# Kernel optimization log

Measured on AMD Instinct MI355X. Metric: run time of the kernel, lower is better.

## Reference

```python
import jax, jax.numpy as jnp
import numpy as np

TEMPERATURE = 8.0  # sqrt(d_k) with d_k = 64
MASK_FILL = -65504.0  # fp16 min, as in the original


def setup_inputs() -> dict:
    key = jax.random.key(0)
    kq, kk, kv, km = jax.random.split(key, 4)
    BH, L, D = 16, 2048, 64
    q = jax.random.normal(kq, (BH, L, D), dtype=jnp.float32)
    k = jax.random.normal(kk, (BH, L, D), dtype=jnp.float32)
    v = jax.random.normal(kv, (BH, L, D), dtype=jnp.float32)
    mask = jax.random.randint(km, (BH, L, L), 0, 2).astype(jnp.bool_)
    return {"q": q, "k": k, "v": v, "mask": mask}


def reference(q, k, v, mask):
    # attn = q @ k^T / temperature, masked_fill, softmax over last dim
    attn = jnp.einsum("bqd,bkd->bqk", q, k) / TEMPERATURE
    attn = jnp.where(mask, MASK_FILL, attn)
    attn = jax.nn.softmax(attn, axis=2)
    # dropout with p=0.0 is identity (eval-mode reference)
    output = jnp.einsum("bqk,bkd->bqd", attn, v)
    return (output, attn)
```

## Files before the change

kernel.cpp:

```cpp
#include <hip/hip_runtime.h>

#define BH 16
#define L 2048
#define D 64
#define QB 32
#define KB 64
#define NKT (L / KB)
#define SCALE 0.125f
#define MASK_FILL -65504.0f

typedef __bf16 bf16x8 __attribute__((ext_vector_type(8)));
typedef float f32x4 __attribute__((ext_vector_type(4)));

__device__ __forceinline__ unsigned f2bf(float f) {
    union { float f; unsigned u; } x; x.f = f;
    return (x.u + 0x7FFFu + ((x.u >> 16) & 1u)) >> 16;
}
__device__ __forceinline__ float bf2f(unsigned short h) {
    union { unsigned u; float f; } x; x.u = ((unsigned)h) << 16;
    return x.f;
}


extern "C" __global__ __launch_bounds__(256)
void preK(const float* __restrict__ k, uint4* __restrict__ wsK)
{
    int idx = blockIdx.x * 256 + threadIdx.x;
    int c   = idx & 7;
    int key = (idx >> 3) & (L - 1);
    int bh  = idx >> 14;
    const float4* src = (const float4*)(k + ((size_t)(bh * L + key) * D + c * 8));
    float4 a = src[0], b = src[1];
    uint4 o;
    o.x = f2bf(a.x) | (f2bf(a.y) << 16);
    o.y = f2bf(a.z) | (f2bf(a.w) << 16);
    o.z = f2bf(b.x) | (f2bf(b.y) << 16);
    o.w = f2bf(b.z) | (f2bf(b.w) << 16);
    wsK[(size_t)(bh * L + key) * 8 + (c ^ (key & 7))] = o;
}

extern "C" __global__ __launch_bounds__(256)
void preV(const float* __restrict__ v, uint4* __restrict__ wsVt)
{
    __shared__ float sT[64 * 68];
    int b = blockIdx.x;
    int bh = b >> 5, kt = b & 31;
    const float4* src = (const float4*)(v + ((size_t)bh * L + kt * 64) * D);
    int t = threadIdx.x;
    #pragma unroll
    for (int i = 0; i < 4; ++i) {
        int i4 = i * 256 + t;
        int key = i4 >> 4, c4 = i4 & 15;
        float4 val = src[i4];
        *(float4*)&sT[key * 68 + c4 * 4] = val;
    }
    __syncthreads();
    int d = t >> 2, cg = t & 3;
    #pragma unroll
    for (int j = 0; j < 2; ++j) {
        int c = cg + j * 4;
        unsigned pk[4];
        #pragma unroll
        for (int e = 0; e < 4; ++e) {
            float x0 = sT[(c * 8 + e * 2    ) * 68 + d];
            float x1 = sT[(c * 8 + e * 2 + 1) * 68 + d];
            pk[e] = f2bf(x0) | (f2bf(x1) << 16);
        }
        wsVt[((size_t)(bh * 32 + kt) * 64 + d) * 8 + (c ^ (d & 7))] =
            make_uint4(pk[0], pk[1], pk[2], pk[3]);
    }
}

extern "C" __global__ __launch_bounds__(256)
void preM(const int* __restrict__ mask, unsigned long long* __restrict__ wsM)
{
    __shared__ unsigned long long sW[16 * 32];
    int b = blockIdx.x;
    size_t row0 = (size_t)b * 16;
    int w = threadIdx.x >> 6, lane = threadIdx.x & 63;
    const int* src = mask + row0 * L;
    for (int rr = 0; rr < 4; ++rr) {
        int r = w * 4 + rr;
        #pragma unroll 8
        for (int wd = 0; wd < 32; ++wd) {
            int val = src[(size_t)r * L + wd * 64 + lane];
            unsigned long long bal = __ballot(val != 0);
            if (lane == 0) sW[r * 32 + wd] = bal;
        }
    }
    __syncthreads();
    int t = threadIdx.x;
    ((uint4*)wsM)[(size_t)b * 256 + t] = ((const uint4*)sW)[t];
}


extern "C" __global__ __launch_bounds__(256, 4)
void sdpa_main(const float* __restrict__ q, const uint4* __restrict__ gKall,
               const uint4* __restrict__ gVall, const unsigned long long* __restrict__ wsM,
               float* __restrict__ out, float* __restrict__ attn)
{
    __shared__ unsigned short sP[2][QB * 72];
    __shared__ float sPart[4][16];

    const int tid = threadIdx.x, lane = tid & 63, w = tid >> 6;
    const int wr = w & 1, wn = w >> 1;
    const int quad = lane >> 4, l15 = lane & 15;
    const int p = blockIdx.x, bh = p & 15, qb = p >> 4, q0 = qb * QB;

    const uint4* gK = gKall + (size_t)bh * L * 8;
    const uint4* gV = gVall + (size_t)bh * L * 8;

    const float* Qp = q + (size_t)(bh * L + q0 + wr * 16 + l15) * D + quad * 8;
    float4 qv0 = *(const float4*)(Qp);
    float4 qv1 = *(const float4*)(Qp + 4);
    float4 qv2 = *(const float4*)(Qp + 32);
    float4 qv3 = *(const float4*)(Qp + 36);
    union { bf16x8 v; unsigned short s[8]; } qa0u, qa1u;
    qa0u.s[0] = f2bf(qv0.x); qa0u.s[1] = f2bf(qv0.y); qa0u.s[2] = f2bf(qv0.z); qa0u.s[3] = f2bf(qv0.w);
    qa0u.s[4] = f2bf(qv1.x); qa0u.s[5] = f2bf(qv1.y); qa0u.s[6] = f2bf(qv1.z); qa0u.s[7] = f2bf(qv1.w);
    qa1u.s[0] = f2bf(qv2.x); qa1u.s[1] = f2bf(qv2.y); qa1u.s[2] = f2bf(qv2.z); qa1u.s[3] = f2bf(qv2.w);
    qa1u.s[4] = f2bf(qv3.x); qa1u.s[5] = f2bf(qv3.y); qa1u.s[6] = f2bf(qv3.z); qa1u.s[7] = f2bf(qv3.w);
    const bf16x8 qa0 = qa0u.v, qa1 = qa1u.v;

    const int key0 = wn * 32 + l15;
    const int key1 = key0 + 16;
    const int s7 = l15 & 7;
    const int o00 = key0 * 8 + ((quad    ) ^ s7);
    const int o01 = key0 * 8 + ((quad + 4) ^ s7);
    const int o10 = key1 * 8 + ((quad    ) ^ s7);
    const int o11 = key1 * 8 + ((quad + 4) ^ s7);

    auto loadK = [&](int kt, bf16x8& a, bf16x8& b, bf16x8& c, bf16x8& d) {
        const uint4* base = gK + (size_t)kt * 512;
        a = *(const bf16x8*)(base + o00);
        b = *(const bf16x8*)(base + o01);
        c = *(const bf16x8*)(base + o10);
        d = *(const bf16x8*)(base + o11);
    };
    auto loadV = [&](int kt, bf16x8& a, bf16x8& b, bf16x8& c, bf16x8& d) {
        const uint4* base = gV + (size_t)kt * 512;
        a = *(const bf16x8*)(base + o00);
        b = *(const bf16x8*)(base + o01);
        c = *(const bf16x8*)(base + o10);
        d = *(const bf16x8*)(base + o11);
    };

    const unsigned long long* Mw = wsM + (size_t)(bh * L + q0 + wr * 16 + quad * 4) * 32;

    unsigned mb[8] = {0u, 0u, 0u, 0u, 0u, 0u, 0u, 0u};

    float lsum[4] = {0.f, 0.f, 0.f, 0.f};

    bf16x8 kA0, kA1, kA2, kA3, kB0, kB1, kB2, kB3;
    loadK(0, kA0, kA1, kA2, kA3);
    loadK(1, kB0, kB1, kB2, kB3);

    for (int kt = 0; kt < NKT; kt += 2) {
        unsigned long long mw0[4], mw1[4];
        #pragma unroll
        for (int r = 0; r < 4; ++r) {
            mw0[r] = Mw[r * 32 + kt];
            mw1[r] = Mw[r * 32 + kt + 1];
        }
        {
            f32x4 acc0 = (f32x4){0.f, 0.f, 0.f, 0.f};
            f32x4 acc1 = (f32x4){0.f, 0.f, 0.f, 0.f};
            acc0 = __builtin_amdgcn_mfma_f32_16x16x32_bf16(qa0, kA0, acc0, 0, 0, 0);
            acc0 = __builtin_amdgcn_mfma_f32_16x16x32_bf16(qa1, kA1, acc0, 0, 0, 0);
            acc1 = __builtin_amdgcn_mfma_f32_16x16x32_bf16(qa0, kA2, acc1, 0, 0, 0);
            acc1 = __builtin_amdgcn_mfma_f32_16x16x32_bf16(qa1, kA3, acc1, 0, 0, 0);
            if (kt + 2 < NKT) loadK(kt + 2, kA0, kA1, kA2, kA3);
            #pragma unroll
            for (int j = 0; j < 2; ++j) {
                const int sh = key0 + j * 16;
                #pragma unroll
                for (int r = 0; r < 4; ++r) {
                    unsigned bit = (unsigned)((mw0[r] >> sh) & 1ull);
                    mb[2 * r + j] |= bit << kt;
                    float e = __expf((j ? acc1[r] : acc0[r]) * SCALE);
                    lsum[r] += bit ? 0.f : e;
                }
            }
        }
        {
            f32x4 acc0 = (f32x4){0.f, 0.f, 0.f, 0.f};
            f32x4 acc1 = (f32x4){0.f, 0.f, 0.f, 0.f};
            acc0 = __builtin_amdgcn_mfma_f32_16x16x32_bf16(qa0, kB0, acc0, 0, 0, 0);
            acc0 = __builtin_amdgcn_mfma_f32_16x16x32_bf16(qa1, kB1, acc0, 0, 0, 0);
            acc1 = __builtin_amdgcn_mfma_f32_16x16x32_bf16(qa0, kB2, acc1, 0, 0, 0);
            acc1 = __builtin_amdgcn_mfma_f32_16x16x32_bf16(qa1, kB3, acc1, 0, 0, 0);
            if (kt + 3 < NKT) loadK(kt + 3, kB0, kB1, kB2, kB3);
            #pragma unroll
            for (int j = 0; j < 2; ++j) {
                const int sh = key0 + j * 16;
                #pragma unroll
                for (int r = 0; r < 4; ++r) {
                    unsigned bit = (unsigned)((mw1[r] >> sh) & 1ull);
                    mb[2 * r + j] |= bit << (kt + 1);
                    float e = __expf((j ? acc1[r] : acc0[r]) * SCALE);
                    lsum[r] += bit ? 0.f : e;
                }
            }
        }
    }

    #pragma unroll
    for (int off = 1; off < 16; off <<= 1)
        #pragma unroll
        for (int r = 0; r < 4; ++r) lsum[r] += __shfl_xor(lsum[r], off, 64);
    if (l15 == 0) {
        #pragma unroll
        for (int r = 0; r < 4; ++r) sPart[w][quad * 4 + r] = lsum[r];
    }
    __syncthreads();
    float rinv[4];
    #pragma unroll
    for (int r = 0; r < 4; ++r)
        rinv[r] = 1.0f / (sPart[wr][quad * 4 + r] + sPart[wr + 2][quad * 4 + r]);

    f32x4 oacc[2];
    oacc[0] = (f32x4){0.f, 0.f, 0.f, 0.f};
    oacc[1] = (f32x4){0.f, 0.f, 0.f, 0.f};
    float* Ab = attn + ((size_t)bh * L + q0) * L;

    bf16x8 k0c, k1c, k2c, k3c;
    loadK(0, k0c, k1c, k2c, k3c);
    for (int kt = 0; kt < NKT; ++kt) {
        bf16x8 v0, v1, v2, v3;
        loadV(kt, v0, v1, v2, v3);

        f32x4 acc0 = (f32x4){0.f, 0.f, 0.f, 0.f};
        f32x4 acc1 = (f32x4){0.f, 0.f, 0.f, 0.f};
        acc0 = __builtin_amdgcn_mfma_f32_16x16x32_bf16(qa0, k0c, acc0, 0, 0, 0);
        acc0 = __builtin_amdgcn_mfma_f32_16x16x32_bf16(qa1, k1c, acc0, 0, 0, 0);
        acc1 = __builtin_amdgcn_mfma_f32_16x16x32_bf16(qa0, k2c, acc1, 0, 0, 0);
        acc1 = __builtin_amdgcn_mfma_f32_16x16x32_bf16(qa1, k3c, acc1, 0, 0, 0);

        unsigned short* sPb = sP[kt & 1];
        #pragma unroll
        for (int j = 0; j < 2; ++j) {
            const int col = key0 + j * 16;
            #pragma unroll
            for (int r = 0; r < 4; ++r) {
                float e = __expf((j ? acc1[r] : acc0[r]) * SCALE);
                float pr = (((mb[2 * r + j] >> kt) & 1u) ? 0.f : e) * rinv[r];
                const int row = wr * 16 + quad * 4 + r;
                Ab[(size_t)row * L + kt * 64 + col] = pr;
                sPb[row * 72 + col] = (unsigned short)f2bf(pr);
            }
        }
        asm volatile("s_waitcnt lgkmcnt(0)\n\ts_barrier" ::: "memory");

        if (kt + 1 < NKT) loadK(kt + 1, k0c, k1c, k2c, k3c);

        const bf16x8 pa0 = *(const bf16x8*)&sPb[(wr * 16 + l15) * 72 + quad * 8];
        const bf16x8 pa1 = *(const bf16x8*)&sPb[(wr * 16 + l15) * 72 + quad * 8 + 32];
        oacc[0] = __builtin_amdgcn_mfma_f32_16x16x32_bf16(pa0, v0, oacc[0], 0, 0, 0);
        oacc[0] = __builtin_amdgcn_mfma_f32_16x16x32_bf16(pa1, v1, oacc[0], 0, 0, 0);
        oacc[1] = __builtin_amdgcn_mfma_f32_16x16x32_bf16(pa0, v2, oacc[1], 0, 0, 0);
        oacc[1] = __builtin_amdgcn_mfma_f32_16x16x32_bf16(pa1, v3, oacc[1], 0, 0, 0);
    }

    float* Ob = out + ((size_t)bh * L + q0) * D;
    #pragma unroll
    for (int j = 0; j < 2; ++j)
        #pragma unroll
        for (int r = 0; r < 4; ++r)
            Ob[(size_t)(wr * 16 + quad * 4 + r) * D + (wn * 2 + j) * 16 + l15] = oacc[j][r];
}


extern "C" __global__ __launch_bounds__(256, 2)
void sdpa_kernel(const float* __restrict__ q, const float* __restrict__ k,
                 const float* __restrict__ v, const int* __restrict__ mask,
                 float* __restrict__ out, float* __restrict__ attn)
{
    __shared__ unsigned short fQ[64 * 72];
    __shared__ unsigned short fK[64 * 72];
    __shared__ unsigned short fVt[64 * 72];
    __shared__ unsigned short fP[64 * 72];
    __shared__ unsigned long long fM[64 * 33];

    const int tid  = threadIdx.x;
    const int lane = tid & 63;
    const int w    = tid >> 6;
    const int quad = lane >> 4;
    const int l15  = lane & 15;

    const int p  = blockIdx.x;
    const int bh = p & (BH - 1);
    const int qb = p >> 4;
    const int q0 = qb * 64;

    const size_t base = (size_t)bh * L * D;
    const float* Qb = q + base + (size_t)q0 * D;
    const float* Kb = k + base;
    const float* Vb = v + base;
    const int*   Mb = mask + (size_t)bh * L * L + (size_t)q0 * L;
    float*       Ab = attn + (size_t)bh * L * L + (size_t)q0 * L;
    float*       Ob = out  + base + (size_t)q0 * D;

    {
        const float2* Qs = (const float2*)Qb;
        for (int i = 0; i < 8; ++i) {
            int idx = i * 256 + tid;
            int row = idx >> 5, d2 = idx & 31;
            float2 val = Qs[idx];
            unsigned pk = f2bf(val.x) | (f2bf(val.y) << 16);
            *(unsigned*)&fQ[row * 72 + d2 * 2] = pk;
        }
    }
    for (int rr = 0; rr < 16; ++rr) {
        int row = w * 16 + rr;
        const int4* Ms = (const int4*)(Mb + (size_t)row * L);
        for (int it = 0; it < 8; ++it) {
            int4 mv = Ms[it * 64 + lane];
            unsigned long long b0 = __ballot(mv.x != 0);
            unsigned long long b1 = __ballot(mv.y != 0);
            unsigned long long b2 = __ballot(mv.z != 0);
            unsigned long long b3 = __ballot(mv.w != 0);
            if (lane == 0) {
                unsigned long long* dst = &fM[row * 33 + it * 4];
                dst[0] = b0; dst[1] = b1; dst[2] = b2; dst[3] = b3;
            }
        }
    }
    __syncthreads();

    const int qrow = w * 16 + l15;
    bf16x8 qa0 = *(const bf16x8*)&fQ[qrow * 72 + quad * 8];
    bf16x8 qa1 = *(const bf16x8*)&fQ[qrow * 72 + quad * 8 + 32];

    float lsum[4] = {0.f, 0.f, 0.f, 0.f};
    for (int kt = 0; kt < 32; ++kt) {
        const int k0 = kt * 64;
        __syncthreads();
        {
            const float2* Ks = (const float2*)(Kb + (size_t)k0 * D);
            for (int i = 0; i < 8; ++i) {
                int idx = i * 256 + tid;
                int row = idx >> 5, d2 = idx & 31;
                float2 val = Ks[idx];
                unsigned pk = f2bf(val.x) | (f2bf(val.y) << 16);
                *(unsigned*)&fK[row * 72 + d2 * 2] = pk;
            }
        }
        __syncthreads();
        f32x4 acc[4];
        for (int nt = 0; nt < 4; ++nt) {
            bf16x8 b0 = *(const bf16x8*)&fK[(nt * 16 + l15) * 72 + quad * 8];
            bf16x8 b1 = *(const bf16x8*)&fK[(nt * 16 + l15) * 72 + quad * 8 + 32];
            f32x4 c = {0.f, 0.f, 0.f, 0.f};
            c = __builtin_amdgcn_mfma_f32_16x16x32_bf16(qa0, b0, c, 0, 0, 0);
            c = __builtin_amdgcn_mfma_f32_16x16x32_bf16(qa1, b1, c, 0, 0, 0);
            acc[nt] = c;
        }
        const int widx = (k0 >> 8) * 4 + (lane & 3);
        const int bsh0 = (k0 >> 2) + (l15 >> 2);
        for (int r = 0; r < 4; ++r) {
            int row = w * 16 + quad * 4 + r;
            unsigned long long mwv = fM[row * 33 + widx];
            float s = 0.f;
            for (int nt = 0; nt < 4; ++nt) {
                float val = acc[nt][r] * SCALE;
                int bit = (int)((mwv >> ((bsh0 + nt * 4) & 63)) & 1ull);
                val = bit ? MASK_FILL : val;
                s += __expf(val);
            }
            lsum[r] += s;
        }
    }
    for (int off = 1; off < 16; off <<= 1)
        for (int r = 0; r < 4; ++r) lsum[r] += __shfl_xor(lsum[r], off, 64);
    float rinv[4];
    for (int r = 0; r < 4; ++r) rinv[r] = 1.0f / lsum[r];

    f32x4 oacc[4];
    for (int nt = 0; nt < 4; ++nt) oacc[nt] = (f32x4){0.f, 0.f, 0.f, 0.f};

    for (int kt = 0; kt < 32; ++kt) {
        const int k0 = kt * 64;
        __syncthreads();
        {
            const float2* Ks = (const float2*)(Kb + (size_t)k0 * D);
            for (int i = 0; i < 8; ++i) {
                int idx = i * 256 + tid;
                int row = idx >> 5, d2 = idx & 31;
                float2 val = Ks[idx];
                unsigned pk = f2bf(val.x) | (f2bf(val.y) << 16);
                *(unsigned*)&fK[row * 72 + d2 * 2] = pk;
            }
        }
        {
            unsigned pk[8];
            for (int jj = 0; jj < 16; ++jj) {
                float val = Vb[(size_t)(k0 + w * 16 + jj) * D + lane];
                unsigned bv = f2bf(val);
                if (jj & 1) pk[jj >> 1] |= bv << 16;
                else        pk[jj >> 1]  = bv;
            }
            uint4* dst = (uint4*)&fVt[lane * 72 + w * 16];
            dst[0] = make_uint4(pk[0], pk[1], pk[2], pk[3]);
            dst[1] = make_uint4(pk[4], pk[5], pk[6], pk[7]);
        }
        __syncthreads();
        f32x4 acc[4];
        for (int nt = 0; nt < 4; ++nt) {
            bf16x8 b0 = *(const bf16x8*)&fK[(nt * 16 + l15) * 72 + quad * 8];
            bf16x8 b1 = *(const bf16x8*)&fK[(nt * 16 + l15) * 72 + quad * 8 + 32];
            f32x4 c = {0.f, 0.f, 0.f, 0.f};
            c = __builtin_amdgcn_mfma_f32_16x16x32_bf16(qa0, b0, c, 0, 0, 0);
            c = __builtin_amdgcn_mfma_f32_16x16x32_bf16(qa1, b1, c, 0, 0, 0);
            acc[nt] = c;
        }
        const int widx = (k0 >> 8) * 4 + (lane & 3);
        const int bsh0 = (k0 >> 2) + (l15 >> 2);
        for (int r = 0; r < 4; ++r) {
            int row = w * 16 + quad * 4 + r;
            unsigned long long mwv = fM[row * 33 + widx];
            for (int nt = 0; nt < 4; ++nt) {
                float val = acc[nt][r] * SCALE;
                int bit = (int)((mwv >> ((bsh0 + nt * 4) & 63)) & 1ull);
                val = bit ? MASK_FILL : val;
                float pr = __expf(val) * rinv[r];
                fP[row * 72 + nt * 16 + l15] = (unsigned short)f2bf(pr);
            }
        }
        for (int it = 0; it < 4; ++it) {
            int row = w * 16 + it * 4 + quad;
            unsigned long long pv = *(const unsigned long long*)&fP[row * 72 + l15 * 4];
            float4 o;
            o.x = bf2f((unsigned short)(pv         & 0xFFFF));
            o.y = bf2f((unsigned short)((pv >> 16) & 0xFFFF));
            o.z = bf2f((unsigned short)((pv >> 32) & 0xFFFF));
            o.w = bf2f((unsigned short)((pv >> 48) & 0xFFFF));
            *(float4*)&Ab[(size_t)row * L + k0 + l15 * 4] = o;
        }
        {
            bf16x8 pa0 = *(const bf16x8*)&fP[qrow * 72 + quad * 8];
            bf16x8 pa1 = *(const bf16x8*)&fP[qrow * 72 + quad * 8 + 32];
            for (int nt = 0; nt < 4; ++nt) {
                bf16x8 vb0 = *(const bf16x8*)&fVt[(nt * 16 + l15) * 72 + quad * 8];
                bf16x8 vb1 = *(const bf16x8*)&fVt[(nt * 16 + l15) * 72 + quad * 8 + 32];
                oacc[nt] = __builtin_amdgcn_mfma_f32_16x16x32_bf16(pa0, vb0, oacc[nt], 0, 0, 0);
                oacc[nt] = __builtin_amdgcn_mfma_f32_16x16x32_bf16(pa1, vb1, oacc[nt], 0, 0, 0);
            }
        }
    }
    for (int nt = 0; nt < 4; ++nt)
        for (int r = 0; r < 4; ++r)
            Ob[(size_t)(w * 16 + quad * 4 + r) * D + nt * 16 + l15] = oacc[nt][r];
}


extern "C" void kernel_launch(void* const* d_in, const int* in_sizes, int n_in,
                              void* d_out, int out_size, void* d_ws, size_t ws_size,
                              hipStream_t stream)
{
    const float* q    = (const float*)d_in[0];
    const float* k    = (const float*)d_in[1];
    const float* v    = (const float*)d_in[2];
    const int*   mask = (const int*)d_in[3];
    float* out  = (float*)d_out;
    float* attn = out + (size_t)BH * L * D;

    const size_t WS_K  = 0;
    const size_t WS_VT = (size_t)BH * L * D * 2;
    const size_t WS_M  = WS_VT + (size_t)BH * L * D * 2;
    const size_t NEED  = WS_M + (size_t)BH * L * 32 * 8;

    if (ws_size >= NEED) {
        uint4* wsK  = (uint4*)((char*)d_ws + WS_K);
        uint4* wsVt = (uint4*)((char*)d_ws + WS_VT);
        unsigned long long* wsM = (unsigned long long*)((char*)d_ws + WS_M);
        hipLaunchKernelGGL(preK, dim3(1024), dim3(256), 0, stream, k, wsK);
        hipLaunchKernelGGL(preV, dim3(512),  dim3(256), 0, stream, v, wsVt);
        hipLaunchKernelGGL(preM, dim3(2048), dim3(256), 0, stream, mask, wsM);
        hipLaunchKernelGGL(sdpa_main, dim3(BH * (L / QB)), dim3(256), 0, stream,
                           q, (const uint4*)wsK, (const uint4*)wsVt, wsM, out, attn);
    } else {
        hipLaunchKernelGGL(sdpa_kernel, dim3(BH * (L / 64)), dim3(256), 0, stream,
                           q, k, v, mask, out, attn);
    }
}
```

Before: 600.5 us.

## Merge preprocessing kernels, widen main blocks to 512 threads, fold scale into Q

The K, V and mask preprocessing kernels are merged into one launch that branches on block index. The main attention kernel moves from 4 to 8 waves per block, so each wave handles 16 keys instead of 32 per tile. The softmax scale is folded into Q before the bf16 conversion, which removes a multiply per score. V loads are now software-pipelined one tile ahead, and the attention matrix, the output and the mask reads use nontemporal hints. In exchange, the larger blocks add barrier cost and the launch bound asks for 8 blocks per CU, which may pressure registers, and pre-scaling Q changes bf16 rounding slightly.

```diff
diff --git a/kernel.cpp b/kernel.cpp
--- a/kernel.cpp
+++ b/kernel.cpp
@@ -21,86 +21,82 @@
     return x.f;
 }
 
-
 extern "C" __global__ __launch_bounds__(256)
-void preK(const float* __restrict__ k, uint4* __restrict__ wsK)
-{
-    int idx = blockIdx.x * 256 + threadIdx.x;
-    int c   = idx & 7;
-    int key = (idx >> 3) & (L - 1);
-    int bh  = idx >> 14;
-    const float4* src = (const float4*)(k + ((size_t)(bh * L + key) * D + c * 8));
-    float4 a = src[0], b = src[1];
-    uint4 o;
-    o.x = f2bf(a.x) | (f2bf(a.y) << 16);
-    o.y = f2bf(a.z) | (f2bf(a.w) << 16);
-    o.z = f2bf(b.x) | (f2bf(b.y) << 16);
-    o.w = f2bf(b.z) | (f2bf(b.w) << 16);
-    wsK[(size_t)(bh * L + key) * 8 + (c ^ (key & 7))] = o;
-}
-
-extern "C" __global__ __launch_bounds__(256)
-void preV(const float* __restrict__ v, uint4* __restrict__ wsVt)
+void prep(const float* __restrict__ k, const float* __restrict__ v,
+          const int* __restrict__ mask,
+          uint4* __restrict__ wsK, uint4* __restrict__ wsVt,
+          unsigned long long* __restrict__ wsM)
 {
     __shared__ float sT[64 * 68];
-    int b = blockIdx.x;
-    int bh = b >> 5, kt = b & 31;
-    const float4* src = (const float4*)(v + ((size_t)bh * L + kt * 64) * D);
-    int t = threadIdx.x;
-    #pragma unroll
-    for (int i = 0; i < 4; ++i) {
-        int i4 = i * 256 + t;
-        int key = i4 >> 4, c4 = i4 & 15;
-        float4 val = src[i4];
-        *(float4*)&sT[key * 68 + c4 * 4] = val;
-    }
-    __syncthreads();
-    int d = t >> 2, cg = t & 3;
-    #pragma unroll
-    for (int j = 0; j < 2; ++j) {
-        int c = cg + j * 4;
-        unsigned pk[4];
-        #pragma unroll
-        for (int e = 0; e < 4; ++e) {
-            float x0 = sT[(c * 8 + e * 2    ) * 68 + d];
-            float x1 = sT[(c * 8 + e * 2 + 1) * 68 + d];
-            pk[e] = f2bf(x0) | (f2bf(x1) << 16);
-        }
-        wsVt[((size_t)(bh * 32 + kt) * 64 + d) * 8 + (c ^ (d & 7))] =
-            make_uint4(pk[0], pk[1], pk[2], pk[3]);
-    }
-}
-
-extern "C" __global__ __launch_bounds__(256)
-void preM(const int* __restrict__ mask, unsigned long long* __restrict__ wsM)
-{
-    __shared__ unsigned long long sW[16 * 32];
-    int b = blockIdx.x;
-    size_t row0 = (size_t)b * 16;
-    int w = threadIdx.x >> 6, lane = threadIdx.x & 63;
-    const int* src = mask + row0 * L;
-    for (int rr = 0; rr < 4; ++rr) {
-        int r = w * 4 + rr;
-        #pragma unroll 8
-        for (int wd = 0; wd < 32; ++wd) {
-            int val = src[(size_t)r * L + wd * 64 + lane];
-            unsigned long long bal = __ballot(val != 0);
-            if (lane == 0) sW[r * 32 + wd] = bal;
-        }
-    }
-    __syncthreads();
-    int t = threadIdx.x;
-    ((uint4*)wsM)[(size_t)b * 256 + t] = ((const uint4*)sW)[t];
-}
-
-
-extern "C" __global__ __launch_bounds__(256, 4)
+    const int b = blockIdx.x;
+    const int t = threadIdx.x;
+
+    if (b < 2048) {
+        unsigned long long* sW = (unsigned long long*)sT;
+        size_t row0 = (size_t)b * 16;
+        int w = t >> 6, lane = t & 63;
+        const int* src = mask + row0 * L;
+        for (int rr = 0; rr < 4; ++rr) {
+            int r = w * 4 + rr;
+            #pragma unroll 8
+            for (int wd = 0; wd < 32; ++wd) {
+                int val = __builtin_nontemporal_load(src + (size_t)r * L + wd * 64 + lane);
+                unsigned long long bal = __ballot(val != 0);
+                if (lane == 0) sW[r * 32 + wd] = bal;
+            }
+        }
+        __syncthreads();
+        ((uint4*)wsM)[(size_t)b * 256 + t] = ((const uint4*)sW)[t];
+    } else if (b < 3072) {
+        int idx = (b - 2048) * 256 + t;
+        int c   = idx & 7;
+        int key = (idx >> 3) & (L - 1);
+        int bh  = idx >> 14;
+        const float4* src = (const float4*)(k + ((size_t)(bh * L + key) * D + c * 8));
+        float4 a = src[0], bb = src[1];
+        uint4 o;
+        o.x = f2bf(a.x)  | (f2bf(a.y)  << 16);
+        o.y = f2bf(a.z)  | (f2bf(a.w)  << 16);
+        o.z = f2bf(bb.x) | (f2bf(bb.y) << 16);
+        o.w = f2bf(bb.z) | (f2bf(bb.w) << 16);
+        wsK[(size_t)(bh * L + key) * 8 + (c ^ (key & 7))] = o;
+    } else {
+        int bb = b - 3072;
+        int bh = bb >> 5, kt = bb & 31;
+        const float4* src = (const float4*)(v + ((size_t)bh * L + kt * 64) * D);
+        #pragma unroll
+        for (int i = 0; i < 4; ++i) {
+            int i4 = i * 256 + t;
+            int key = i4 >> 4, c4 = i4 & 15;
+            float4 val = src[i4];
+            *(float4*)&sT[key * 68 + c4 * 4] = val;
+        }
+        __syncthreads();
+        int d = t >> 2, cg = t & 3;
+        #pragma unroll
+        for (int j = 0; j < 2; ++j) {
+            int c = cg + j * 4;
+            unsigned pk[4];
+            #pragma unroll
+            for (int e = 0; e < 4; ++e) {
+                float x0 = sT[(c * 8 + e * 2    ) * 68 + d];
+                float x1 = sT[(c * 8 + e * 2 + 1) * 68 + d];
+                pk[e] = f2bf(x0) | (f2bf(x1) << 16);
+            }
+            wsVt[((size_t)(bh * 32 + kt) * 64 + d) * 8 + (c ^ (d & 7))] =
+                make_uint4(pk[0], pk[1], pk[2], pk[3]);
+        }
+    }
+}
+
+
+extern "C" __global__ __launch_bounds__(512, 8)
 void sdpa_main(const float* __restrict__ q, const uint4* __restrict__ gKall,
                const uint4* __restrict__ gVall, const unsigned long long* __restrict__ wsM,
                float* __restrict__ out, float* __restrict__ attn)
 {
     __shared__ unsigned short sP[2][QB * 72];
-    __shared__ float sPart[4][16];
+    __shared__ float sPart[8][16];
 
     const int tid = threadIdx.x, lane = tid & 63, w = tid >> 6;
     const int wr = w & 1, wn = w >> 1;
@@ -116,44 +112,41 @@
     float4 qv2 = *(const float4*)(Qp + 32);
     float4 qv3 = *(const float4*)(Qp + 36);
     union { bf16x8 v; unsigned short s[8]; } qa0u, qa1u;
-    qa0u.s[0] = f2bf(qv0.x); qa0u.s[1] = f2bf(qv0.y); qa0u.s[2] = f2bf(qv0.z); qa0u.s[3] = f2bf(qv0.w);
-    qa0u.s[4] = f2bf(qv1.x); qa0u.s[5] = f2bf(qv1.y); qa0u.s[6] = f2bf(qv1.z); qa0u.s[7] = f2bf(qv1.w);
-    qa1u.s[0] = f2bf(qv2.x); qa1u.s[1] = f2bf(qv2.y); qa1u.s[2] = f2bf(qv2.z); qa1u.s[3] = f2bf(qv2.w);
-    qa1u.s[4] = f2bf(qv3.x); qa1u.s[5] = f2bf(qv3.y); qa1u.s[6] = f2bf(qv3.z); qa1u.s[7] = f2bf(qv3.w);
+    qa0u.s[0] = f2bf(qv0.x * SCALE); qa0u.s[1] = f2bf(qv0.y * SCALE);
+    qa0u.s[2] = f2bf(qv0.z * SCALE); qa0u.s[3] = f2bf(qv0.w * SCALE);
+    qa0u.s[4] = f2bf(qv1.x * SCALE); qa0u.s[5] = f2bf(qv1.y * SCALE);
+    qa0u.s[6] = f2bf(qv1.z * SCALE); qa0u.s[7] = f2bf(qv1.w * SCALE);
+    qa1u.s[0] = f2bf(qv2.x * SCALE); qa1u.s[1] = f2bf(qv2.y * SCALE);
+    qa1u.s[2] = f2bf(qv2.z * SCALE); qa1u.s[3] = f2bf(qv2.w * SCALE);
+    qa1u.s[4] = f2bf(qv3.x * SCALE); qa1u.s[5] = f2bf(qv3.y * SCALE);
+    qa1u.s[6] = f2bf(qv3.z * SCALE); qa1u.s[7] = f2bf(qv3.w * SCALE);
     const bf16x8 qa0 = qa0u.v, qa1 = qa1u.v;
 
-    const int key0 = wn * 32 + l15;
-    const int key1 = key0 + 16;
+    const int key = wn * 16 + l15;
     const int s7 = l15 & 7;
-    const int o00 = key0 * 8 + ((quad    ) ^ s7);
-    const int o01 = key0 * 8 + ((quad + 4) ^ s7);
-    const int o10 = key1 * 8 + ((quad    ) ^ s7);
-    const int o11 = key1 * 8 + ((quad + 4) ^ s7);
-
-    auto loadK = [&](int kt, bf16x8& a, bf16x8& b, bf16x8& c, bf16x8& d) {
+    const int oA = key * 8 + ((quad    ) ^ s7);
+    const int oB = key * 8 + ((quad + 4) ^ s7);
+
+    auto loadK = [&](int kt, bf16x8& a, bf16x8& b) {
         const uint4* base = gK + (size_t)kt * 512;
-        a = *(const bf16x8*)(base + o00);
-        b = *(const bf16x8*)(base + o01);
-        c = *(const bf16x8*)(base + o10);
-        d = *(const bf16x8*)(base + o11);
+        a = *(const bf16x8*)(base + oA);
+        b = *(const bf16x8*)(base + oB);
     };
-    auto loadV = [&](int kt, bf16x8& a, bf16x8& b, bf16x8& c, bf16x8& d) {
+    auto loadV = [&](int kt, bf16x8& a, bf16x8& b) {
         const uint4* base = gV + (size_t)kt * 512;
-        a = *(const bf16x8*)(base + o00);
-        b = *(const bf16x8*)(base + o01);
-        c = *(const bf16x8*)(base + o10);
-        d = *(const bf16x8*)(base + o11);
+        a = *(const bf16x8*)(base + oA);
+        b = *(const bf16x8*)(base + oB);
     };
 
     const unsigned long long* Mw = wsM + (size_t)(bh * L + q0 + wr * 16 + quad * 4) * 32;
 
-    unsigned mb[8] = {0u, 0u, 0u, 0u, 0u, 0u, 0u, 0u};
+    unsigned mb[4] = {0u, 0u, 0u, 0u};
 
     float lsum[4] = {0.f, 0.f, 0.f, 0.f};
 
-    bf16x8 kA0, kA1, kA2, kA3, kB0, kB1, kB2, kB3;
-    loadK(0, kA0, kA1, kA2, kA3);
-    loadK(1, kB0, kB1, kB2, kB3);
+    bf16x8 kA0, kA1, kB0, kB1;
+    loadK(0, kA0, kA1);
+    loadK(1, kB0, kB1);
 
     for (int kt = 0; kt < NKT; kt += 2) {
         unsigned long long mw0[4], mw1[4];
@@ -163,43 +156,29 @@
             mw1[r] = Mw[r * 32 + kt + 1];
         }
         {
-            f32x4 acc0 = (f32x4){0.f, 0.f, 0.f, 0.f};
-            f32x4 acc1 = (f32x4){0.f, 0.f, 0.f, 0.f};
-            acc0 = __builtin_amdgcn_mfma_f32_16x16x32_bf16(qa0, kA0, acc0, 0, 0, 0);
-            acc0 = __builtin_amdgcn_mfma_f32_16x16x32_bf16(qa1, kA1, acc0, 0, 0, 0);
-            acc1 = __builtin_amdgcn_mfma_f32_16x16x32_bf16(qa0, kA2, acc1, 0, 0, 0);
-            acc1 = __builtin_amdgcn_mfma_f32_16x16x32_bf16(qa1, kA3, acc1, 0, 0, 0);
-            if (kt + 2 < NKT) loadK(kt + 2, kA0, kA1, kA2, kA3);
+            f32x4 acc = (f32x4){0.f, 0.f, 0.f, 0.f};
+            acc = __builtin_amdgcn_mfma_f32_16x16x32_bf16(qa0, kA0, acc, 0, 0, 0);
+            acc = __builtin_amdgcn_mfma_f32_16x16x32_bf16(qa1, kA1, acc, 0, 0, 0);
+            if (kt + 2 < NKT) loadK(kt + 2, kA0, kA1);
             #pragma unroll
-            for (int j = 0; j < 2; ++j) {
-                const int sh = key0 + j * 16;
-                #pragma unroll
-                for (int r = 0; r < 4; ++r) {
-                    unsigned bit = (unsigned)((mw0[r] >> sh) & 1ull);
-                    mb[2 * r + j] |= bit << kt;
-                    float e = __expf((j ? acc1[r] : acc0[r]) * SCALE);
-                    lsum[r] += bit ? 0.f : e;
-                }
-            }
-        }
-        {
-            f32x4 acc0 = (f32x4){0.f, 0.f, 0.f, 0.f};
-            f32x4 acc1 = (f32x4){0.f, 0.f, 0.f, 0.f};
-            acc0 = __builtin_amdgcn_mfma_f32_16x16x32_bf16(qa0, kB0, acc0, 0, 0, 0);
-            acc0 = __builtin_amdgcn_mfma_f32_16x16x32_bf16(qa1, kB1, acc0, 0, 0, 0);
-            acc1 = __builtin_amdgcn_mfma_f32_16x16x32_bf16(qa0, kB2, acc1, 0, 0, 0);
-            acc1 = __builtin_amdgcn_mfma_f32_16x16x32_bf16(qa1, kB3, acc1, 0, 0, 0);
-            if (kt + 3 < NKT) loadK(kt + 3, kB0, kB1, kB2, kB3);
+            for (int r = 0; r < 4; ++r) {
+                unsigned bit = (unsigned)((mw0[r] >> key) & 1ull);
+                mb[r] |= bit << kt;
+                float e = __expf(acc[r]);
+                lsum[r] += bit ? 0.f : e;
+            }
+        }
+        {
+            f32x4 acc = (f32x4){0.f, 0.f, 0.f, 0.f};
+            acc = __builtin_amdgcn_mfma_f32_16x16x32_bf16(qa0, kB0, acc, 0, 0, 0);
+            acc = __builtin_amdgcn_mfma_f32_16x16x32_bf16(qa1, kB1, acc, 0, 0, 0);
+            if (kt + 3 < NKT) loadK(kt + 3, kB0, kB1);
             #pragma unroll
-            for (int j = 0; j < 2; ++j) {
-                const int sh = key0 + j * 16;
-                #pragma unroll
-                for (int r = 0; r < 4; ++r) {
-                    unsigned bit = (unsigned)((mw1[r] >> sh) & 1ull);
-                    mb[2 * r + j] |= bit << (kt + 1);
-                    float e = __expf((j ? acc1[r] : acc0[r]) * SCALE);
-                    lsum[r] += bit ? 0.f : e;
-                }
+            for (int r = 0; r < 4; ++r) {
+                unsigned bit = (unsigned)((mw1[r] >> key) & 1ull);
+                mb[r] |= bit << (kt + 1);
+                float e = __expf(acc[r]);
+                lsum[r] += bit ? 0.f : e;
             }
         }
     }
@@ -216,57 +195,45 @@
     float rinv[4];
     #pragma unroll
     for (int r = 0; r < 4; ++r)
-        rinv[r] = 1.0f / (sPart[wr][quad * 4 + r] + sPart[wr + 2][quad * 4 + r]);
-
-    f32x4 oacc[2];
-    oacc[0] = (f32x4){0.f, 0.f, 0.f, 0.f};
-    oacc[1] = (f32x4){0.f, 0.f, 0.f, 0.f};
+        rinv[r] = 1.0f / (sPart[wr][quad * 4 + r] + sPart[wr + 2][quad * 4 + r] +
+                          sPart[wr + 4][quad * 4 + r] + sPart[wr + 6][quad * 4 + r]);
+
+    f32x4 oacc = (f32x4){0.f, 0.f, 0.f, 0.f};
     float* Ab = attn + ((size_t)bh * L + q0) * L;
 
-    bf16x8 k0c, k1c, k2c, k3c;
-    loadK(0, k0c, k1c, k2c, k3c);
+    bf16x8 k0c, k1c, v0c, v1c;
+    loadK(0, k0c, k1c);
+    loadV(0, v0c, v1c);
     for (int kt = 0; kt < NKT; ++kt) {
-        bf16x8 v0, v1, v2, v3;
-        loadV(kt, v0, v1, v2, v3);
-
-        f32x4 acc0 = (f32x4){0.f, 0.f, 0.f, 0.f};
-        f32x4 acc1 = (f32x4){0.f, 0.f, 0.f, 0.f};
-        acc0 = __builtin_amdgcn_mfma_f32_16x16x32_bf16(qa0, k0c, acc0, 0, 0, 0);
-        acc0 = __builtin_amdgcn_mfma_f32_16x16x32_bf16(qa1, k1c, acc0, 0, 0, 0);
-        acc1 = __builtin_amdgcn_mfma_f32_16x16x32_bf16(qa0, k2c, acc1, 0, 0, 0);
-        acc1 = __builtin_amdgcn_mfma_f32_16x16x32_bf16(qa1, k3c, acc1, 0, 0, 0);
+        f32x4 acc = (f32x4){0.f, 0.f, 0.f, 0.f};
+        acc = __builtin_amdgcn_mfma_f32_16x16x32_bf16(qa0, k0c, acc, 0, 0, 0);
+        acc = __builtin_amdgcn_mfma_f32_16x16x32_bf16(qa1, k1c, acc, 0, 0, 0);
 
         unsigned short* sPb = sP[kt & 1];
         #pragma unroll
-        for (int j = 0; j < 2; ++j) {
-            const int col = key0 + j * 16;
-            #pragma unroll
-            for (int r = 0; r < 4; ++r) {
-                float e = __expf((j ? acc1[r] : acc0[r]) * SCALE);
-                float pr = (((mb[2 * r + j] >> kt) & 1u) ? 0.f : e) * rinv[r];
-                const int row = wr * 16 + quad * 4 + r;
-                Ab[(size_t)row * L + kt * 64 + col] = pr;
-                sPb[row * 72 + col] = (unsigned short)f2bf(pr);
-            }
+        for (int r = 0; r < 4; ++r) {
+            float e = __expf(acc[r]);
+            float pr = (((mb[r] >> kt) & 1u) ? 0.f : e) * rinv[r];
+            const int row = wr * 16 + quad * 4 + r;
+            __builtin_nontemporal_store(pr, &Ab[(size_t)row * L + kt * 64 + key]);
+            sPb[row * 72 + key] = (unsigned short)f2bf(pr);
         }
         asm volatile("s_waitcnt lgkmcnt(0)\n\ts_barrier" ::: "memory");
 
-        if (kt + 1 < NKT) loadK(kt + 1, k0c, k1c, k2c, k3c);
+        if (kt + 1 < NKT) loadK(kt + 1, k0c, k1c);
 
         const bf16x8 pa0 = *(const bf16x8*)&sPb[(wr * 16 + l15) * 72 + quad * 8];
         const bf16x8 pa1 = *(const bf16x8*)&sPb[(wr * 16 + l15) * 72 + quad * 8 + 32];
-        oacc[0] = __builtin_amdgcn_mfma_f32_16x16x32_bf16(pa0, v0, oacc[0], 0, 0, 0);
-        oacc[0] = __builtin_amdgcn_mfma_f32_16x16x32_bf16(pa1, v1, oacc[0], 0, 0, 0);
-        oacc[1] = __builtin_amdgcn_mfma_f32_16x16x32_bf16(pa0, v2, oacc[1], 0, 0, 0);
-        oacc[1] = __builtin_amdgcn_mfma_f32_16x16x32_bf16(pa1, v3, oacc[1], 0, 0, 0);
+        oacc = __builtin_amdgcn_mfma_f32_16x16x32_bf16(pa0, v0c, oacc, 0, 0, 0);
+        oacc = __builtin_amdgcn_mfma_f32_16x16x32_bf16(pa1, v1c, oacc, 0, 0, 0);
+        if (kt + 1 < NKT) loadV(kt + 1, v0c, v1c);
     }
 
     float* Ob = out + ((size_t)bh * L + q0) * D;
     #pragma unroll
-    for (int j = 0; j < 2; ++j)
-        #pragma unroll
-        for (int r = 0; r < 4; ++r)
-            Ob[(size_t)(wr * 16 + quad * 4 + r) * D + (wn * 2 + j) * 16 + l15] = oacc[j][r];
+    for (int r = 0; r < 4; ++r)
+        __builtin_nontemporal_store(oacc[r],
+            &Ob[(size_t)(wr * 16 + quad * 4 + r) * D + key]);
 }
 
 
@@ -473,10 +440,9 @@
         uint4* wsK  = (uint4*)((char*)d_ws + WS_K);
         uint4* wsVt = (uint4*)((char*)d_ws + WS_VT);
         unsigned long long* wsM = (unsigned long long*)((char*)d_ws + WS_M);
-        hipLaunchKernelGGL(preK, dim3(1024), dim3(256), 0, stream, k, wsK);
-        hipLaunchKernelGGL(preV, dim3(512),  dim3(256), 0, stream, v, wsVt);
-        hipLaunchKernelGGL(preM, dim3(2048), dim3(256), 0, stream, mask, wsM);
-        hipLaunchKernelGGL(sdpa_main, dim3(BH * (L / QB)), dim3(256), 0, stream,
+        hipLaunchKernelGGL(prep, dim3(3584), dim3(256), 0, stream,
+                           k, v, mask, wsK, wsVt, wsM);
+        hipLaunchKernelGGL(sdpa_main, dim3(BH * (L / QB)), dim3(512), 0, stream,
                            q, (const uint4*)wsK, (const uint4*)wsVt, wsM, out, attn);
     } else {
         hipLaunchKernelGGL(sdpa_kernel, dim3(BH * (L / 64)), dim3(256), 0, stream,
```

After: 662.6 us. 1.1x slower.
